# Performance work log

Hardware: AMD Instinct MI355X
Metric: run time of the kernel (lower is better)

## Reference

```python
import jax, jax.numpy as jnp
import numpy as np

B, T, D = 4096, 256, 64          # batch, steps, state_dim
LD, CD = 4, 8                    # latent_dim, categorical_dim
H = 32                           # mlp_hidden
FEAT = D + LD * CD               # fc1 input dim


def setup_inputs() -> dict:
    key = jax.random.key(0)
    ks = jax.random.split(key, 8)
    states = jax.random.normal(ks[0], (B, T, D), dtype=jnp.float32)
    # pre-sampled Gumbel(0,1) noise, as used inside F.gumbel_softmax
    u = jax.random.uniform(ks[1], (B, T, LD, CD), jnp.float32, 1e-6, 1.0 - 1e-6)
    gumbel = -jnp.log(-jnp.log(u))
    tau = jnp.float32(1.0)
    def lin(k, fan_in, fan_out):
        bound = 1.0 / np.sqrt(fan_in)
        kw, kb = jax.random.split(k)
        W = jax.random.uniform(kw, (fan_in, fan_out), jnp.float32, -bound, bound)
        b = jax.random.uniform(kb, (fan_out,), jnp.float32, -bound, bound)
        return W, b
    W1, b1 = lin(ks[2], FEAT, H)
    W2, b2 = lin(ks[3], H, H)
    W3, b3 = lin(ks[4], H, LD * CD)
    return {"states": states, "gumbel": gumbel, "tau": tau,
            "W1": W1, "b1": b1, "W2": W2, "b2": b2, "W3": W3, "b3": b3}


def reference(states, gumbel, tau, W1, b1, W2, b2, W3, b3):
    Bs, T, _ = states.shape
    ld, cd = gumbel.shape[2], gumbel.shape[3]
    # init_states: eye(cd)[0] tiled latent_dim times -> [B, ld*cd]
    c0 = jnp.tile(jax.nn.one_hot(0, cd, dtype=states.dtype), (Bs, ld))
    xs = (jnp.swapaxes(states, 0, 1), jnp.swapaxes(gumbel, 0, 1))  # [T,B,...]

    def step(c, x):
        s, g = x                                   # s:[B,D], g:[B,ld,cd]
        z = jnp.concatenate([s, c], axis=-1)       # [B, FEAT]
        h1 = jax.nn.relu(z @ W1 + b1)
        h2 = jax.nn.relu(h1 @ W2 + b2)
        q = (h2 @ W3 + b3).reshape(Bs, ld, cd)
        y_soft = jax.nn.softmax((q + g) / tau, axis=-1)
        # hard=True (eval mode) straight-through one-hot
        y_hard = jax.nn.one_hot(jnp.argmax(y_soft, axis=-1), cd, dtype=y_soft.dtype)
        y = y_hard + y_soft - jax.lax.stop_gradient(y_soft)
        c_new = y.reshape(Bs, ld * cd)
        return c_new, c_new

    _, out = jax.lax.scan(step, c0, xs)            # [T, B, ld*cd]
    return jnp.swapaxes(out, 0, 1)                 # [B, T, ld*cd]
```

## Files before the change

### kernel.cpp

```cpp
#include <hip/hip_runtime.h>

#define NB   4096
#define NT   256
#define ND   64
#define CT   16
#define NCH  (NT / CT)

__device__ __forceinline__ float ror16(float x) {
  return __int_as_float(__builtin_amdgcn_update_dpp(
      0, __float_as_int(x), 0x121 , 0xF, 0xF, false));
}

#define SWZ(x, patt) __int_as_float(__builtin_amdgcn_ds_swizzle(__float_as_int(x), (patt)))
#define SWZ_X1(x) SWZ(x, 0x041F)
#define SWZ_X2(x) SWZ(x, 0x081F)
#define SWZ_X4(x) SWZ(x, 0x101F)

#define ROTMAC(WA, WB, WC, WD)                          \
  _Pragma("unroll")                                     \
  for (int r = 0; r < 16; ++r) {                        \
    a0 = fmaf(vl, WA[r], a0);                           \
    a1 = fmaf(vh, WB[r], a1);                           \
    a2 = fmaf(vl, WC[r], a2);                           \
    a3 = fmaf(vh, WD[r], a3);                           \
    if (r < 15) { vl = ror16(vl); vh = ror16(vh); }     \
  }

__global__ __launch_bounds__(256, 1)
void enc_kernel(const float* __restrict__ S,
                const float* __restrict__ G,
                const float* __restrict__ W1,
                const float* __restrict__ b1,
                const float* __restrict__ W2,
                const float* __restrict__ b2,
                const float* __restrict__ W3,
                const float* __restrict__ b3,
                float* __restrict__ out) {
  __shared__ float ldsH[4][64][33];

  const int tid  = threadIdx.x;
  const int wave = tid >> 6;
  const int lane = tid & 63;
  const int bw   = lane >> 4;
  const int s    = lane & 15;
  const int b    = blockIdx.x * 16 + wave * 4 + bw;

  float w1A[16], w1B[16], w1C[16], w1D[16];
  float w2A[16], w2B[16], w2C[16], w2D[16];
  float w3A[16], w3B[16], w3C[16], w3D[16];
#pragma unroll
  for (int r = 0; r < 16; ++r) {
    const int klo = (s - r) & 15;
    const int khi = klo + 16;
    w1A[r] = W1[(64 + klo) * 32 + s];
    w1B[r] = W1[(64 + khi) * 32 + s];
    w1C[r] = W1[(64 + klo) * 32 + s + 16];
    w1D[r] = W1[(64 + khi) * 32 + s + 16];
    w2A[r] = W2[klo * 32 + s];
    w2B[r] = W2[khi * 32 + s];
    w2C[r] = W2[klo * 32 + s + 16];
    w2D[r] = W2[khi * 32 + s + 16];
    w3A[r] = W3[klo * 32 + s];
    w3B[r] = W3[khi * 32 + s];
    w3C[r] = W3[klo * 32 + s + 16];
    w3D[r] = W3[khi * 32 + s + 16];
  }
  const float b2l = b2[s], b2h = b2[s + 16];
  const float b3l = b3[s], b3h = b3[s + 16];

  float clo = (s == 0 || s == 8) ? 1.f : 0.f;
  float chi = clo;

  const size_t gbase = ((size_t)b * NT) * 32 + s;
  float gA0 = G[gbase + 0 * 32], gA1 = G[gbase + 0 * 32 + 16];
  float gB0 = G[gbase + 1 * 32], gB1 = G[gbase + 1 * 32 + 16];

  float* outp = out + ((size_t)b * NT) * 32 + s;
  float* myrow = &ldsH[wave][lane][0];
  const int rbase = bw * 16;

#pragma unroll 1
  for (int ch = 0; ch < NCH; ++ch) {
    {
      const float* srow = S + ((size_t)b * NT + (ch * CT + s)) * ND;
      float4 xs[16];
#pragma unroll
      for (int i = 0; i < 16; ++i) xs[i] = ((const float4*)srow)[i];
      float acc[32];
#pragma unroll
      for (int j = 0; j < 32; ++j) acc[j] = 0.f;
#pragma unroll
      for (int k4 = 0; k4 < 16; ++k4) {
        const float xv[4] = {xs[k4].x, xs[k4].y, xs[k4].z, xs[k4].w};
#pragma unroll
        for (int kk = 0; kk < 4; ++kk) {
          const int k = k4 * 4 + kk;
          const float xk = xv[kk];
#pragma unroll
          for (int j = 0; j < 32; ++j)
            acc[j] = fmaf(xk, W1[k * 32 + j], acc[j]);
        }
      }
#pragma unroll
      for (int j = 0; j < 32; ++j) myrow[j] = acc[j] + b1[j];
    }

    float h1c0 = ldsH[wave][rbase + 0][s];
    float h1c1 = ldsH[wave][rbase + 0][s + 16];
#pragma unroll 1
    for (int tc = 0; tc < CT; ++tc) {
      const int t = ch * CT + tc;
      const int tn = (tc < CT - 1) ? tc + 1 : tc;
      const float h1n0 = ldsH[wave][rbase + tn][s];
      const float h1n1 = ldsH[wave][rbase + tn][s + 16];
      const int tg = (t + 2 < NT) ? t + 2 : NT - 1;
      const float gC0 = G[gbase + (size_t)tg * 32];
      const float gC1 = G[gbase + (size_t)tg * 32 + 16];

      float a0 = h1c0, a1 = 0.f, a2 = h1c1, a3 = 0.f;
      float vl = clo, vh = chi;
      ROTMAC(w1A, w1B, w1C, w1D)
      float hl = fmaxf(a0 + a1, 0.f);
      float hh = fmaxf(a2 + a3, 0.f);

      a0 = b2l; a1 = 0.f; a2 = b2h; a3 = 0.f; vl = hl; vh = hh;
      ROTMAC(w2A, w2B, w2C, w2D)
      hl = fmaxf(a0 + a1, 0.f);
      hh = fmaxf(a2 + a3, 0.f);

      a0 = b3l + gA0; a1 = 0.f; a2 = b3h + gA1; a3 = 0.f; vl = hl; vh = hh;
      ROTMAC(w3A, w3B, w3C, w3D)
      const float q0 = a0 + a1;
      const float q1 = a2 + a3;

      float m0 = q0, m1 = q1;
      m0 = fmaxf(m0, SWZ_X1(m0)); m1 = fmaxf(m1, SWZ_X1(m1));
      m0 = fmaxf(m0, SWZ_X2(m0)); m1 = fmaxf(m1, SWZ_X2(m1));
      m0 = fmaxf(m0, SWZ_X4(m0)); m1 = fmaxf(m1, SWZ_X4(m1));
      const unsigned long long bl0 = __ballot(q0 == m0);
      const unsigned long long bl1 = __ballot(q1 == m1);
      const int sh = lane & 56;
      const unsigned gr0 = (unsigned)(bl0 >> sh) & 255u;
      const unsigned gr1 = (unsigned)(bl1 >> sh) & 255u;
      const int my = lane & 7;
      const float y0 = ((__ffs(gr0) - 1) == my) ? 1.f : 0.f;
      const float y1 = ((__ffs(gr1) - 1) == my) ? 1.f : 0.f;

      outp[(size_t)t * 32]      = y0;
      outp[(size_t)t * 32 + 16] = y1;

      clo = y0; chi = y1;
      h1c0 = h1n0; h1c1 = h1n1;
      gA0 = gB0; gA1 = gB1; gB0 = gC0; gB1 = gC1;
    }
  }
}

extern "C" void kernel_launch(void* const* d_in, const int* in_sizes, int n_in,
                              void* d_out, int out_size, void* d_ws, size_t ws_size,
                              hipStream_t stream) {
  const float* S  = (const float*)d_in[0];
  const float* G  = (const float*)d_in[1];
  const float* W1 = (const float*)d_in[3];
  const float* b1 = (const float*)d_in[4];
  const float* W2 = (const float*)d_in[5];
  const float* b2 = (const float*)d_in[6];
  const float* W3 = (const float*)d_in[7];
  const float* b3 = (const float*)d_in[8];
  float* out = (float*)d_out;

  hipLaunchKernelGGL(enc_kernel, dim3(NB / 16), dim3(256), 0, stream,
                     S, G, W1, b1, W2, b2, W3, b3, out);
}
```

Baseline: 809.9 us.

## Split state projection into a parallel pre-kernel, reuse output buffer for it

The non-recurrent S@W1+b1 projection moves out of the recurrent kernel into its own fully parallel kernel (one thread per row). That kernel writes into the output buffer, and the recurrent kernel then reads those values two steps ahead before overwriting each slot with the one-hot result. The intent is to take the large matmul off the low-occupancy serial kernel and drop the LDS staging. The argmax max-reduction also switches from ds_swizzle to DPP ops. The cost is an extra launch and a global write plus read of the hidden buffer.

Measured after the change: 777.1 us. -4.0%, faster.

```diff
diff --git a/kernel.cpp b/kernel.cpp
--- a/kernel.cpp
+++ b/kernel.cpp
@@ -3,18 +3,19 @@
 #define NB   4096
 #define NT   256
 #define ND   64
-#define CT   16
-#define NCH  (NT / CT)
 
-__device__ __forceinline__ float ror16(float x) {
+template <int CTRL>
+__device__ __forceinline__ float dppf(float x) {
   return __int_as_float(__builtin_amdgcn_update_dpp(
-      0, __float_as_int(x), 0x121 , 0xF, 0xF, false));
+      0, __float_as_int(x), CTRL, 0xF, 0xF, false));
 }
-
-#define SWZ(x, patt) __int_as_float(__builtin_amdgcn_ds_swizzle(__float_as_int(x), (patt)))
-#define SWZ_X1(x) SWZ(x, 0x041F)
-#define SWZ_X2(x) SWZ(x, 0x081F)
-#define SWZ_X4(x) SWZ(x, 0x101F)
+#define ROR16(x) dppf<0x121>(x)
+__device__ __forceinline__ float max8(float x) {
+  float t = fmaxf(x, dppf<0xB1>(x));
+  t = fmaxf(t, dppf<0x4E>(t));
+  t = fmaxf(t, dppf<0x141>(t));
+  return t;
+}
 
 #define ROTMAC(WA, WB, WC, WD)                          \
   _Pragma("unroll")                                     \
@@ -23,21 +24,55 @@
     a1 = fmaf(vh, WB[r], a1);                           \
     a2 = fmaf(vl, WC[r], a2);                           \
     a3 = fmaf(vh, WD[r], a3);                           \
-    if (r < 15) { vl = ror16(vl); vh = ror16(vh); }     \
+    if (r < 15) { vl = ROR16(vl); vh = ROR16(vh); }     \
   }
 
+__global__ __launch_bounds__(256)
+void h1pre_kernel(const float* __restrict__ S,
+                  const float* __restrict__ W1,
+                  const float* __restrict__ b1,
+                  float* __restrict__ out) {
+  const int row = blockIdx.x * 256 + threadIdx.x;
+  const float4* srow = (const float4*)(S + (size_t)row * ND);
+
+  float acc[32];
+#pragma unroll
+  for (int j = 0; j < 32; ++j) acc[j] = b1[j];
+
+#pragma unroll
+  for (int kc = 0; kc < 4; ++kc) {
+    float4 x[4];
+#pragma unroll
+    for (int i = 0; i < 4; ++i) x[i] = srow[kc * 4 + i];
+#pragma unroll
+    for (int i = 0; i < 4; ++i) {
+      const float xv[4] = {x[i].x, x[i].y, x[i].z, x[i].w};
+#pragma unroll
+      for (int kk = 0; kk < 4; ++kk) {
+        const int k = kc * 16 + i * 4 + kk;
+        const float xk = xv[kk];
+#pragma unroll
+        for (int j = 0; j < 32; ++j)
+          acc[j] = fmaf(xk, W1[k * 32 + j], acc[j]);
+      }
+    }
+  }
+
+  float4* orow = (float4*)(out + (size_t)row * 32);
+#pragma unroll
+  for (int j4 = 0; j4 < 8; ++j4)
+    orow[j4] = make_float4(acc[4 * j4], acc[4 * j4 + 1],
+                           acc[4 * j4 + 2], acc[4 * j4 + 3]);
+}
+
 __global__ __launch_bounds__(256, 1)
-void enc_kernel(const float* __restrict__ S,
-                const float* __restrict__ G,
+void rec_kernel(const float* __restrict__ G,
                 const float* __restrict__ W1,
-                const float* __restrict__ b1,
                 const float* __restrict__ W2,
                 const float* __restrict__ b2,
                 const float* __restrict__ W3,
                 const float* __restrict__ b3,
                 float* __restrict__ out) {
-  __shared__ float ldsH[4][64][33];
-
   const int tid  = threadIdx.x;
   const int wave = tid >> 6;
   const int lane = tid & 63;
@@ -72,87 +107,53 @@
   float chi = clo;
 
   const size_t gbase = ((size_t)b * NT) * 32 + s;
+  const size_t obase = ((size_t)b * NT) * 32 + s;
   float gA0 = G[gbase + 0 * 32], gA1 = G[gbase + 0 * 32 + 16];
   float gB0 = G[gbase + 1 * 32], gB1 = G[gbase + 1 * 32 + 16];
-
-  float* outp = out + ((size_t)b * NT) * 32 + s;
-  float* myrow = &ldsH[wave][lane][0];
-  const int rbase = bw * 16;
+  float hA0 = out[obase + 0 * 32], hA1 = out[obase + 0 * 32 + 16];
+  float hB0 = out[obase + 1 * 32], hB1 = out[obase + 1 * 32 + 16];
 
 #pragma unroll 1
-  for (int ch = 0; ch < NCH; ++ch) {
-    {
-      const float* srow = S + ((size_t)b * NT + (ch * CT + s)) * ND;
-      float4 xs[16];
-#pragma unroll
-      for (int i = 0; i < 16; ++i) xs[i] = ((const float4*)srow)[i];
-      float acc[32];
-#pragma unroll
-      for (int j = 0; j < 32; ++j) acc[j] = 0.f;
-#pragma unroll
-      for (int k4 = 0; k4 < 16; ++k4) {
-        const float xv[4] = {xs[k4].x, xs[k4].y, xs[k4].z, xs[k4].w};
-#pragma unroll
-        for (int kk = 0; kk < 4; ++kk) {
-          const int k = k4 * 4 + kk;
-          const float xk = xv[kk];
-#pragma unroll
-          for (int j = 0; j < 32; ++j)
-            acc[j] = fmaf(xk, W1[k * 32 + j], acc[j]);
-        }
-      }
-#pragma unroll
-      for (int j = 0; j < 32; ++j) myrow[j] = acc[j] + b1[j];
-    }
+  for (int t = 0; t < NT; ++t) {
+    const int tp = (t + 2 < NT) ? t + 2 : NT - 1;
+    const float hC0 = out[obase + (size_t)tp * 32];
+    const float hC1 = out[obase + (size_t)tp * 32 + 16];
+    const float gC0 = G[gbase + (size_t)tp * 32];
+    const float gC1 = G[gbase + (size_t)tp * 32 + 16];
 
-    float h1c0 = ldsH[wave][rbase + 0][s];
-    float h1c1 = ldsH[wave][rbase + 0][s + 16];
-#pragma unroll 1
-    for (int tc = 0; tc < CT; ++tc) {
-      const int t = ch * CT + tc;
-      const int tn = (tc < CT - 1) ? tc + 1 : tc;
-      const float h1n0 = ldsH[wave][rbase + tn][s];
-      const float h1n1 = ldsH[wave][rbase + tn][s + 16];
-      const int tg = (t + 2 < NT) ? t + 2 : NT - 1;
-      const float gC0 = G[gbase + (size_t)tg * 32];
-      const float gC1 = G[gbase + (size_t)tg * 32 + 16];
+    float a0 = hA0, a1 = 0.f, a2 = hA1, a3 = 0.f;
+    float vl = clo, vh = chi;
+    ROTMAC(w1A, w1B, w1C, w1D)
+    float hl = fmaxf(a0 + a1, 0.f);
+    float hh = fmaxf(a2 + a3, 0.f);
 
-      float a0 = h1c0, a1 = 0.f, a2 = h1c1, a3 = 0.f;
-      float vl = clo, vh = chi;
-      ROTMAC(w1A, w1B, w1C, w1D)
-      float hl = fmaxf(a0 + a1, 0.f);
-      float hh = fmaxf(a2 + a3, 0.f);
+    a0 = b2l; a1 = 0.f; a2 = b2h; a3 = 0.f; vl = hl; vh = hh;
+    ROTMAC(w2A, w2B, w2C, w2D)
+    hl = fmaxf(a0 + a1, 0.f);
+    hh = fmaxf(a2 + a3, 0.f);
 
-      a0 = b2l; a1 = 0.f; a2 = b2h; a3 = 0.f; vl = hl; vh = hh;
-      ROTMAC(w2A, w2B, w2C, w2D)
-      hl = fmaxf(a0 + a1, 0.f);
-      hh = fmaxf(a2 + a3, 0.f);
+    a0 = b3l + gA0; a1 = 0.f; a2 = b3h + gA1; a3 = 0.f; vl = hl; vh = hh;
+    ROTMAC(w3A, w3B, w3C, w3D)
+    const float q0 = a0 + a1;
+    const float q1 = a2 + a3;
 
-      a0 = b3l + gA0; a1 = 0.f; a2 = b3h + gA1; a3 = 0.f; vl = hl; vh = hh;
-      ROTMAC(w3A, w3B, w3C, w3D)
-      const float q0 = a0 + a1;
-      const float q1 = a2 + a3;
+    const float m0 = max8(q0);
+    const float m1 = max8(q1);
+    const unsigned long long bl0 = __ballot(q0 == m0);
+    const unsigned long long bl1 = __ballot(q1 == m1);
+    const int sh = lane & 56;
+    const unsigned gr0 = (unsigned)(bl0 >> sh) & 255u;
+    const unsigned gr1 = (unsigned)(bl1 >> sh) & 255u;
+    const int my = lane & 7;
+    const float y0 = ((__ffs(gr0) - 1) == my) ? 1.f : 0.f;
+    const float y1 = ((__ffs(gr1) - 1) == my) ? 1.f : 0.f;
 
-      float m0 = q0, m1 = q1;
-      m0 = fmaxf(m0, SWZ_X1(m0)); m1 = fmaxf(m1, SWZ_X1(m1));
-      m0 = fmaxf(m0, SWZ_X2(m0)); m1 = fmaxf(m1, SWZ_X2(m1));
-      m0 = fmaxf(m0, SWZ_X4(m0)); m1 = fmaxf(m1, SWZ_X4(m1));
-      const unsigned long long bl0 = __ballot(q0 == m0);
-      const unsigned long long bl1 = __ballot(q1 == m1);
-      const int sh = lane & 56;
-      const unsigned gr0 = (unsigned)(bl0 >> sh) & 255u;
-      const unsigned gr1 = (unsigned)(bl1 >> sh) & 255u;
-      const int my = lane & 7;
-      const float y0 = ((__ffs(gr0) - 1) == my) ? 1.f : 0.f;
-      const float y1 = ((__ffs(gr1) - 1) == my) ? 1.f : 0.f;
+    out[obase + (size_t)t * 32]      = y0;
+    out[obase + (size_t)t * 32 + 16] = y1;
 
-      outp[(size_t)t * 32]      = y0;
-      outp[(size_t)t * 32 + 16] = y1;
-
-      clo = y0; chi = y1;
-      h1c0 = h1n0; h1c1 = h1n1;
-      gA0 = gB0; gA1 = gB1; gB0 = gC0; gB1 = gC1;
-    }
+    clo = y0; chi = y1;
+    hA0 = hB0; hA1 = hB1; hB0 = hC0; hB1 = hC1;
+    gA0 = gB0; gA1 = gB1; gB0 = gC0; gB1 = gC1;
   }
 }
 
@@ -169,6 +170,8 @@
   const float* b3 = (const float*)d_in[8];
   float* out = (float*)d_out;
 
-  hipLaunchKernelGGL(enc_kernel, dim3(NB / 16), dim3(256), 0, stream,
-                     S, G, W1, b1, W2, b2, W3, b3, out);
+  hipLaunchKernelGGL(h1pre_kernel, dim3((NB * NT) / 256), dim3(256), 0, stream,
+                     S, W1, b1, out);
+  hipLaunchKernelGGL(rec_kernel, dim3(NB / 16), dim3(256), 0, stream,
+                     G, W1, W2, b2, W3, b3, out);
 }
```
